# Optimization experiments

Measured on AMD Instinct MI355X. Metric: run time of the kernel, lower is better.

Reference implementation:

```python
import jax, jax.numpy as jnp
import numpy as np

B, N, C = 32, 16384, 256
D, H, S = 64, 128, 7
ITERS = 3
EPS = 1e-6
SCALE = D ** -0.5


def _ln(x, g, b):
    m = jnp.mean(x, axis=-1, keepdims=True)
    v = jnp.var(x, axis=-1, keepdims=True)
    return (x - m) / jnp.sqrt(v + 1e-5) * g + b


def _gru(x, h, Wih, Whh, bih, bhh):
    # PyTorch GRUCell: Wih/Whh are [3D, D]
    gi = x @ Wih.T + bih
    gh = h @ Whh.T + bhh
    ir, iz, inn = jnp.split(gi, 3, axis=-1)
    hr, hz, hn = jnp.split(gh, 3, axis=-1)
    r = jax.nn.sigmoid(ir + hr)
    z = jax.nn.sigmoid(iz + hz)
    n = jnp.tanh(inn + r * hn)
    return (1.0 - z) * n + z * h


def setup_inputs() -> dict:
    key = jax.random.key(0)
    ks = jax.random.split(key, 20)
    s_c = C ** -0.5
    s_d = D ** -0.5
    s_h = H ** -0.5
    p = {}
    p["inputs"] = jax.random.normal(ks[0], (B, N, C), jnp.float32)
    p["slots_mu"] = jax.random.normal(ks[1], (B, S, D), jnp.float32)
    p["ln_in_g"] = jnp.ones((C,), jnp.float32)
    p["ln_in_b"] = jnp.zeros((C,), jnp.float32)
    p["Wk"] = jax.random.normal(ks[2], (C, D), jnp.float32) * s_c
    p["Wv"] = jax.random.normal(ks[3], (C, D), jnp.float32) * s_c
    p["q_ln_g"] = jnp.ones((D,), jnp.float32)
    p["q_ln_b"] = jnp.zeros((D,), jnp.float32)
    p["Wq"] = jax.random.normal(ks[4], (D, D), jnp.float32) * s_d
    p["bq_ln_g"] = jnp.ones((D,), jnp.float32)
    p["bq_ln_b"] = jnp.zeros((D,), jnp.float32)
    p["bWq"] = jax.random.normal(ks[5], (D, D), jnp.float32) * s_d
    p["gru_Wih"] = jax.random.normal(ks[6], (3 * D, D), jnp.float32) * s_d
    p["gru_Whh"] = jax.random.normal(ks[7], (3 * D, D), jnp.float32) * s_d
    p["gru_bih"] = jnp.zeros((3 * D,), jnp.float32)
    p["gru_bhh"] = jnp.zeros((3 * D,), jnp.float32)
    p["mlp_ln_g"] = jnp.ones((D,), jnp.float32)
    p["mlp_ln_b"] = jnp.zeros((D,), jnp.float32)
    p["mlp_W1"] = jax.random.normal(ks[8], (D, H), jnp.float32) * s_d
    p["mlp_b1"] = jnp.zeros((H,), jnp.float32)
    p["mlp_W2"] = jax.random.normal(ks[9], (H, D), jnp.float32) * s_h
    p["mlp_b2"] = jnp.zeros((D,), jnp.float32)
    p["bmlp_ln_g"] = jnp.ones((D,), jnp.float32)
    p["bmlp_ln_b"] = jnp.zeros((D,), jnp.float32)
    p["bmlp_W1"] = jax.random.normal(ks[10], (D, H), jnp.float32) * s_d
    p["bmlp_b1"] = jnp.zeros((H,), jnp.float32)
    p["bmlp_W2"] = jax.random.normal(ks[11], (H, D), jnp.float32) * s_h
    p["bmlp_b2"] = jnp.zeros((D,), jnp.float32)
    return p


def reference(inputs, slots_mu, ln_in_g, ln_in_b, Wk, Wv, q_ln_g, q_ln_b, Wq,
              bq_ln_g, bq_ln_b, bWq, gru_Wih, gru_Whh, gru_bih, gru_bhh,
              mlp_ln_g, mlp_ln_b, mlp_W1, mlp_b1, mlp_W2, mlp_b2,
              bmlp_ln_g, bmlp_ln_b, bmlp_W1, bmlp_b1, bmlp_W2, bmlp_b2):
    x = _ln(inputs, ln_in_g, ln_in_b)          # [B,N,C]
    k = x @ Wk                                  # [B,N,D]
    v = x @ Wv                                  # [B,N,D]
    fg = slots_mu[:, :-1]                       # [B,S-1,D]
    bg = slots_mu[:, -1:]                       # [B,1,D]
    for _ in range(ITERS):
        fg_prev, bg_prev = fg, bg
        fq = _ln(fg, q_ln_g, q_ln_b) @ Wq
        bq = _ln(bg, bq_ln_g, bq_ln_b) @ bWq
        q = jnp.concatenate([fq, bq], axis=1)   # [B,S,D]
        logits = SCALE * jnp.einsum('bnd,bmd->bnm', k, q)  # [B,N,S]
        attn = jax.nn.softmax(logits, axis=-1) + EPS
        fa = attn[..., :-1]
        ba = attn[..., -1:]
        fa = fa / jnp.sum(fa, axis=1, keepdims=True)
        ba = ba / jnp.sum(ba, axis=1, keepdims=True)
        fu = jnp.einsum('bnm,bnd->bmd', fa, v)  # [B,S-1,D]
        bu = jnp.einsum('bnm,bnd->bmd', ba, v)  # [B,1,D]
        fg = _gru(fu.reshape(-1, D), fg_prev.reshape(-1, D),
                  gru_Wih, gru_Whh, gru_bih, gru_bhh).reshape(B, S - 1, D)
        fg = fg + (jax.nn.relu(_ln(fg, mlp_ln_g, mlp_ln_b) @ mlp_W1 + mlp_b1) @ mlp_W2 + mlp_b2)
        # NOTE: original code uses self.gru (shared) for bg, not bg_gru
        bg = _gru(bu.reshape(-1, D), bg_prev.reshape(-1, D),
                  gru_Wih, gru_Whh, gru_bih, gru_bhh).reshape(B, 1, D)
        bg = bg + (jax.nn.relu(_ln(bg, bmlp_ln_g, bmlp_ln_b) @ bmlp_W1 + bmlp_b1) @ bmlp_W2 + bmlp_b2)
    return jnp.concatenate([fg, bg], axis=1)    # [B,S,D]
```

## Files before the change

### kernel.cpp

```cpp
#include <hip/hip_runtime.h>
#include <hip/hip_bf16.h>

typedef __bf16 bf16_t;
typedef __bf16 bf16x4 __attribute__((ext_vector_type(4)));
typedef __bf16 bf16x8 __attribute__((ext_vector_type(8)));
typedef float f32x4 __attribute__((ext_vector_type(4)));

#define B_ 32
#define N_ 16384
#define C_ 256
#define D_ 64
#define ROWS_TOTAL (B_ * N_)

__device__ inline float wave_sum64(float v) {
#pragma unroll
  for (int o = 1; o < 64; o <<= 1) v += __shfl_xor(v, o);
  return v;
}

__device__ inline float sigmoidf_(float x) { return 1.0f / (1.0f + __expf(-x)); }
__device__ inline float tanhf_(float x) { return 1.0f - 2.0f / (__expf(2.0f * x) + 1.0f); }

__global__ __launch_bounds__(256) void prep_kernel(
    const float* __restrict__ Wk, const float* __restrict__ Wv,
    const float* __restrict__ Wih, const float* __restrict__ Whh,
    const float* __restrict__ slots, bf16_t* __restrict__ Wb,
    float* __restrict__ WihT, float* __restrict__ WhhT, float* __restrict__ g) {
  int i = blockIdx.x * 256 + threadIdx.x;
  if (i < 32768) {
    int j = i & 7, l = (i >> 3) & 63, t = (i >> 9) & 7, kb = i >> 12;
    int k = kb * 32 + (l >> 4) * 8 + j;
    int n = t * 16 + (l & 15);
    float v = (n < 64) ? Wk[k * 64 + n] : Wv[k * 64 + (n - 64)];
    Wb[i] = (bf16_t)v;
  } else if (i < 45056) {
    int idx = i - 32768;
    int c = idx / 192, j = idx % 192;
    WihT[idx] = Wih[j * 64 + c];
  } else if (i < 57344) {
    int idx = i - 45056;
    int c = idx / 192, j = idx % 192;
    WhhT[idx] = Whh[j * 64 + c];
  } else if (i < 71680) {
    int idx = i - 57344;
    g[idx] = slots[idx];
  }
}

__global__ __launch_bounds__(64) void qk_kernel(
    const float* __restrict__ g, const float* __restrict__ qg,
    const float* __restrict__ qb, const float* __restrict__ Wq,
    const float* __restrict__ bqg, const float* __restrict__ bqb,
    const float* __restrict__ bWq, float* __restrict__ q,
    float* __restrict__ acc, float* __restrict__ wsum) {
  __shared__ float sx[64];
  int bid = blockIdx.x, lane = threadIdx.x;
  int m = bid % 7;
  const float* lng = (m < 6) ? qg : bqg;
  const float* lnb = (m < 6) ? qb : bqb;
  const float* W = (m < 6) ? Wq : bWq;
  float gvv = g[bid * 64 + lane];
  float s = wave_sum64(gvv);
  float s2 = wave_sum64(gvv * gvv);
  float mean = s * (1.0f / 64.0f);
  float var = s2 * (1.0f / 64.0f) - mean * mean;
  float rstd = rsqrtf(var + 1e-5f);
  sx[lane] = (gvv - mean) * rstd * lng[lane] + lnb[lane];
  __syncthreads();
  float qd = 0.0f;
#pragma unroll 8
  for (int c = 0; c < 64; ++c) qd += sx[c] * W[c * 64 + lane];
  q[bid * 64 + lane] = qd;
  acc[bid * 64 + lane] = 0.0f;
  if (lane == 0) wsum[bid] = 0.0f;
}

__global__ __launch_bounds__(512) void proj_ln_kernel(
    const float* __restrict__ inp, const float* __restrict__ lng,
    const float* __restrict__ lnb, const bf16_t* __restrict__ Wb,
    bf16_t* __restrict__ kbuf, bf16_t* __restrict__ vbuf,
    const float* __restrict__ q, float* __restrict__ acc_g,
    float* __restrict__ wsum_g) {
  __shared__ bf16_t xs[128 * 256];
  __shared__ float qs[448];
  __shared__ float s_acc[448];
  __shared__ float s_w[7];
  const int tid = threadIdx.x, w = tid >> 6, lane = tid & 63;
  const int q4 = lane >> 4, lp = lane & 15;
  const long row0 = (long)blockIdx.x * 128;
  const int b = (int)(row0 >> 14);

  for (int idx = tid; idx < 448; idx += 512) {
    qs[idx] = q[b * 448 + idx];
    s_acc[idx] = 0.0f;
  }
  if (tid < 7) s_w[tid] = 0.0f;

  float4 gv[4], bv[4];
#pragma unroll
  for (int j = 0; j < 4; ++j) {
    gv[j] = *(const float4*)(lng + lp * 16 + j * 4);
    bv[j] = *(const float4*)(lnb + lp * 16 + j * 4);
  }

#pragma unroll
  for (int i = 0; i < 4; ++i) {
    int r = w * 16 + i * 4 + q4;
    const float* rp = inp + (row0 + r) * C_ + lp * 16;
    float4 x0 = *(const float4*)(rp);
    float4 x1 = *(const float4*)(rp + 4);
    float4 x2 = *(const float4*)(rp + 8);
    float4 x3 = *(const float4*)(rp + 12);
    float s = (x0.x + x0.y + x0.z + x0.w) + (x1.x + x1.y + x1.z + x1.w) +
              (x2.x + x2.y + x2.z + x2.w) + (x3.x + x3.y + x3.z + x3.w);
    float s2 = (x0.x * x0.x + x0.y * x0.y + x0.z * x0.z + x0.w * x0.w) +
               (x1.x * x1.x + x1.y * x1.y + x1.z * x1.z + x1.w * x1.w) +
               (x2.x * x2.x + x2.y * x2.y + x2.z * x2.z + x2.w * x2.w) +
               (x3.x * x3.x + x3.y * x3.y + x3.z * x3.z + x3.w * x3.w);
#pragma unroll
    for (int o = 1; o < 16; o <<= 1) {
      s += __shfl_xor(s, o);
      s2 += __shfl_xor(s2, o);
    }
    float mean = s * (1.0f / 256.0f);
    float var = s2 * (1.0f / 256.0f) - mean * mean;
    float rstd = rsqrtf(var + 1e-5f);
    bf16x8 y0, y1;
    y0[0] = (bf16_t)((x0.x - mean) * rstd * gv[0].x + bv[0].x);
    y0[1] = (bf16_t)((x0.y - mean) * rstd * gv[0].y + bv[0].y);
    y0[2] = (bf16_t)((x0.z - mean) * rstd * gv[0].z + bv[0].z);
    y0[3] = (bf16_t)((x0.w - mean) * rstd * gv[0].w + bv[0].w);
    y0[4] = (bf16_t)((x1.x - mean) * rstd * gv[1].x + bv[1].x);
    y0[5] = (bf16_t)((x1.y - mean) * rstd * gv[1].y + bv[1].y);
    y0[6] = (bf16_t)((x1.z - mean) * rstd * gv[1].z + bv[1].z);
    y0[7] = (bf16_t)((x1.w - mean) * rstd * gv[1].w + bv[1].w);
    y1[0] = (bf16_t)((x2.x - mean) * rstd * gv[2].x + bv[2].x);
    y1[1] = (bf16_t)((x2.y - mean) * rstd * gv[2].y + bv[2].y);
    y1[2] = (bf16_t)((x2.z - mean) * rstd * gv[2].z + bv[2].z);
    y1[3] = (bf16_t)((x2.w - mean) * rstd * gv[2].w + bv[2].w);
    y1[4] = (bf16_t)((x3.x - mean) * rstd * gv[3].x + bv[3].x);
    y1[5] = (bf16_t)((x3.y - mean) * rstd * gv[3].y + bv[3].y);
    y1[6] = (bf16_t)((x3.z - mean) * rstd * gv[3].z + bv[3].z);
    y1[7] = (bf16_t)((x3.w - mean) * rstd * gv[3].w + bv[3].w);
    int base = r * 32, swz = r & 31;
    *(bf16x8*)(xs + (size_t)(base + ((2 * lp) ^ swz)) * 8) = y0;
    *(bf16x8*)(xs + (size_t)(base + ((2 * lp + 1) ^ swz)) * 8) = y1;
  }
  __syncthreads();

  f32x4 acc[8];
  const f32x4 zf = {0.0f, 0.0f, 0.0f, 0.0f};
#pragma unroll
  for (int t = 0; t < 8; ++t) acc[t] = zf;

  const int r0 = w * 16 + lp;
  const int rsw = r0 & 31;
  for (int kb = 0; kb < 8; ++kb) {
    bf16x8 a = *(const bf16x8*)(xs + (size_t)(r0 * 32 + ((kb * 4 + q4) ^ rsw)) * 8);
#pragma unroll
    for (int t = 0; t < 8; ++t) {
      bf16x8 bfr = *(const bf16x8*)(Wb + (size_t)((kb * 8 + t) * 64 + lane) * 8);
      acc[t] = __builtin_amdgcn_mfma_f32_16x16x32_bf16(a, bfr, acc[t], 0, 0, 0);
    }
  }

#pragma unroll
  for (int t = 0; t < 8; ++t) {
    bf16_t* dst = (t < 4) ? kbuf : vbuf;
    int c = (t & 3) * 16 + lp;
#pragma unroll
    for (int reg = 0; reg < 4; ++reg) {
      long gr = row0 + w * 16 + q4 * 4 + reg;
      dst[gr * 64 + c] = (bf16_t)acc[t][reg];
    }
  }

  float av[7][4];
  float wa[7];
#pragma unroll
  for (int m = 0; m < 7; ++m) {
    wa[m] = 0.0f;
#pragma unroll
    for (int t = 0; t < 4; ++t) av[m][t] = 0.0f;
  }

#pragma unroll
  for (int reg = 0; reg < 4; ++reg) {
    float p[7];
#pragma unroll
    for (int m = 0; m < 7; ++m) p[m] = 0.0f;
#pragma unroll
    for (int t = 0; t < 4; ++t) {
      float at = acc[t][reg];
#pragma unroll
      for (int m = 0; m < 7; ++m) p[m] += at * qs[m * 64 + t * 16 + lp];
    }
#pragma unroll
    for (int m = 0; m < 7; ++m) {
      p[m] += __shfl_xor(p[m], 1);
      p[m] += __shfl_xor(p[m], 2);
      p[m] += __shfl_xor(p[m], 4);
      p[m] += __shfl_xor(p[m], 8);
    }
    float mx = -1e30f;
#pragma unroll
    for (int m = 0; m < 7; ++m) {
      p[m] *= 0.125f;
      mx = fmaxf(mx, p[m]);
    }
    float s = 0.0f;
#pragma unroll
    for (int m = 0; m < 7; ++m) {
      p[m] = __expf(p[m] - mx);
      s += p[m];
    }
    float inv = 1.0f / s;
#pragma unroll
    for (int m = 0; m < 7; ++m) {
      float a = p[m] * inv + 1e-6f;
      wa[m] += a;
#pragma unroll
      for (int t = 0; t < 4; ++t) av[m][t] += a * acc[4 + t][reg];
    }
  }

#pragma unroll
  for (int m = 0; m < 7; ++m) {
#pragma unroll
    for (int t = 0; t < 4; ++t) {
      av[m][t] += __shfl_xor(av[m][t], 16);
      av[m][t] += __shfl_xor(av[m][t], 32);
    }
    wa[m] += __shfl_xor(wa[m], 16);
    wa[m] += __shfl_xor(wa[m], 32);
  }
  if (q4 == 0) {
#pragma unroll
    for (int m = 0; m < 7; ++m)
#pragma unroll
      for (int t = 0; t < 4; ++t)
        atomicAdd(&s_acc[m * 64 + t * 16 + lp], av[m][t]);
  }
  if (lane == 0) {
#pragma unroll
    for (int m = 0; m < 7; ++m) atomicAdd(&s_w[m], wa[m]);
  }
  __syncthreads();
  for (int idx = tid; idx < 448; idx += 512)
    atomicAdd(&acc_g[b * 448 + idx], s_acc[idx]);
  if (tid < 7) atomicAdd(&wsum_g[b * 7 + tid], s_w[tid]);
}

__global__ __launch_bounds__(256) void attend_kernel(
    const bf16_t* __restrict__ kbuf, const bf16_t* __restrict__ vbuf,
    const float* __restrict__ q, float* __restrict__ acc,
    float* __restrict__ wsum) {
  __shared__ float qs[448];
  __shared__ float s_acc[448];
  __shared__ float s_w[7];
  int tid = threadIdx.x, w = tid >> 6, lane = tid & 63;
  int g4 = lane >> 4, lp = lane & 15;
  long chunk0 = (long)blockIdx.x * 512;
  int b = (int)(chunk0 >> 14);

  for (int idx = tid; idx < 448; idx += 256) {
    qs[idx] = q[b * 448 + idx];
    s_acc[idx] = 0.0f;
  }
  if (tid < 7) s_w[tid] = 0.0f;
  __syncthreads();

  float4 qv[7];
  const float4* qs4 = (const float4*)qs;
#pragma unroll
  for (int m = 0; m < 7; ++m) qv[m] = qs4[m * 16 + lp];

  float av[7][4];
  float wa[7];
#pragma unroll
  for (int m = 0; m < 7; ++m) {
    wa[m] = 0.0f;
#pragma unroll
    for (int j = 0; j < 4; ++j) av[m][j] = 0.0f;
  }

  for (int it = 0; it < 32; ++it) {
    long row = chunk0 + it * 16 + w * 4 + g4;
    bf16x4 kv = *(const bf16x4*)(kbuf + row * 64 + lp * 4);
    bf16x4 vv = *(const bf16x4*)(vbuf + row * 64 + lp * 4);
    float k0 = kv[0], k1 = kv[1], k2 = kv[2], k3 = kv[3];
    float lg[7];
#pragma unroll
    for (int m = 0; m < 7; ++m)
      lg[m] = k0 * qv[m].x + k1 * qv[m].y + k2 * qv[m].z + k3 * qv[m].w;
#pragma unroll
    for (int m = 0; m < 7; ++m) {
      lg[m] += __shfl_xor(lg[m], 1);
      lg[m] += __shfl_xor(lg[m], 2);
      lg[m] += __shfl_xor(lg[m], 4);
      lg[m] += __shfl_xor(lg[m], 8);
    }
    float mx = -1e30f;
#pragma unroll
    for (int m = 0; m < 7; ++m) {
      lg[m] *= 0.125f;
      mx = fmaxf(mx, lg[m]);
    }
    float e[7], s = 0.0f;
#pragma unroll
    for (int m = 0; m < 7; ++m) {
      e[m] = __expf(lg[m] - mx);
      s += e[m];
    }
    float inv = 1.0f / s;
    float v0 = vv[0], v1 = vv[1], v2 = vv[2], v3 = vv[3];
#pragma unroll
    for (int m = 0; m < 7; ++m) {
      float a = e[m] * inv + 1e-6f;
      wa[m] += a;
      av[m][0] += a * v0;
      av[m][1] += a * v1;
      av[m][2] += a * v2;
      av[m][3] += a * v3;
    }
  }

#pragma unroll
  for (int m = 0; m < 7; ++m) {
#pragma unroll
    for (int j = 0; j < 4; ++j) {
      av[m][j] += __shfl_xor(av[m][j], 16);
      av[m][j] += __shfl_xor(av[m][j], 32);
    }
    wa[m] += __shfl_xor(wa[m], 16);
    wa[m] += __shfl_xor(wa[m], 32);
  }
  if (g4 == 0) {
#pragma unroll
    for (int m = 0; m < 7; ++m)
#pragma unroll
      for (int j = 0; j < 4; ++j) atomicAdd(&s_acc[m * 64 + lp * 4 + j], av[m][j]);
  }
  if (lane == 0) {
#pragma unroll
    for (int m = 0; m < 7; ++m) atomicAdd(&s_w[m], wa[m]);
  }
  __syncthreads();
  for (int idx = tid; idx < 448; idx += 256) atomicAdd(&acc[b * 448 + idx], s_acc[idx]);
  if (tid < 7) atomicAdd(&wsum[b * 7 + tid], s_w[tid]);
}

__global__ __launch_bounds__(192) void update_kernel(
    const float* __restrict__ acc, const float* __restrict__ wsum,
    const float* __restrict__ g, const float* __restrict__ WihT,
    const float* __restrict__ WhhT, const float* __restrict__ bih,
    const float* __restrict__ bhh, const float* __restrict__ mlg,
    const float* __restrict__ mlb, const float* __restrict__ mW1,
    const float* __restrict__ mb1, const float* __restrict__ mW2,
    const float* __restrict__ mb2, const float* __restrict__ bmlg,
    const float* __restrict__ bmlb, const float* __restrict__ bW1,
    const float* __restrict__ bb1, const float* __restrict__ bW2,
    const float* __restrict__ bb2, float* __restrict__ gout,
    const float* __restrict__ qg, const float* __restrict__ qb,
    const float* __restrict__ Wq, const float* __restrict__ bqg,
    const float* __restrict__ bqb, const float* __restrict__ bWq,
    float* __restrict__ qout, float* __restrict__ accz,
    float* __restrict__ wsz, int write_q) {
  __shared__ float fu[64], hp[64], gi[192], gh[192], h2[64], xb[64], a1[128], go[64];
  int tid = threadIdx.x, bid = blockIdx.x, m = bid % 7;

  const float *lg_, *lb_, *W1_, *b1_, *W2_, *b2_;
  if (m < 6) { lg_ = mlg; lb_ = mlb; W1_ = mW1; b1_ = mb1; W2_ = mW2; b2_ = mb2; }
  else       { lg_ = bmlg; lb_ = bmlb; W1_ = bW1; b1_ = bb1; W2_ = bW2; b2_ = bb2; }

  if (tid < 64) {
    float wv = wsum[bid];
    fu[tid] = acc[bid * 64 + tid] / wv;
    hp[tid] = g[bid * 64 + tid];
  }
  __syncthreads();

  {
    int j = tid;
    float a = bih[j], bsum = bhh[j];
    for (int c = 0; c < 64; ++c) {
      a += fu[c] * WihT[c * 192 + j];
      bsum += hp[c] * WhhT[c * 192 + j];
    }
    gi[j] = a;
    gh[j] = bsum;
  }
  __syncthreads();

  if (tid < 64) {
    int d = tid;
    float r = sigmoidf_(gi[d] + gh[d]);
    float z = sigmoidf_(gi[64 + d] + gh[64 + d]);
    float n = tanhf_(gi[128 + d] + r * gh[128 + d]);
    float h = (1.0f - z) * n + z * hp[d];
    h2[d] = h;
    float s = wave_sum64(h);
    float s2 = wave_sum64(h * h);
    float mean = s * (1.0f / 64.0f);
    float var = s2 * (1.0f / 64.0f) - mean * mean;
    xb[d] = (h - mean) * rsqrtf(var + 1e-5f) * lg_[d] + lb_[d];
  }
  __syncthreads();

  if (tid < 128) {
    int hh = tid;
    float a = b1_[hh];
    for (int c = 0; c < 64; ++c) a += xb[c] * W1_[c * 128 + hh];
    a1[hh] = fmaxf(a, 0.0f);
  }
  __syncthreads();

  if (tid < 64) {
    int d = tid;
    float o = b2_[d];
    for (int hh = 0; hh < 128; ++hh) o += a1[hh] * W2_[hh * 64 + d];
    float res = h2[d] + o;
    gout[bid * 64 + d] = res;
    go[d] = res;
  }
  __syncthreads();

  if (write_q) {
    if (tid < 64) {
      const float* qlng = (m < 6) ? qg : bqg;
      const float* qlnb = (m < 6) ? qb : bqb;
      const float* W = (m < 6) ? Wq : bWq;
      float gvv = go[tid];
      float s = wave_sum64(gvv);
      float s2 = wave_sum64(gvv * gvv);
      float mean = s * (1.0f / 64.0f);
      float var = s2 * (1.0f / 64.0f) - mean * mean;
      xb[tid] = (gvv - mean) * rsqrtf(var + 1e-5f) * qlng[tid] + qlnb[tid];
      __syncwarp();
      float qd = 0.0f;
      const float* Wl = W;
#pragma unroll 8
      for (int c = 0; c < 64; ++c) qd += xb[c] * Wl[c * 64 + tid];
      qout[bid * 64 + tid] = qd;
      accz[bid * 64 + tid] = 0.0f;
      if (tid == 0) wsz[bid] = 0.0f;
    }
  }
}

extern "C" void kernel_launch(void* const* d_in, const int* in_sizes, int n_in,
                              void* d_out, int out_size, void* d_ws, size_t ws_size,
                              hipStream_t stream) {
  const float* inputs   = (const float*)d_in[0];
  const float* slots_mu = (const float*)d_in[1];
  const float* ln_in_g  = (const float*)d_in[2];
  const float* ln_in_b  = (const float*)d_in[3];
  const float* Wk       = (const float*)d_in[4];
  const float* Wv       = (const float*)d_in[5];
  const float* q_ln_g   = (const float*)d_in[6];
  const float* q_ln_b   = (const float*)d_in[7];
  const float* Wq       = (const float*)d_in[8];
  const float* bq_ln_g  = (const float*)d_in[9];
  const float* bq_ln_b  = (const float*)d_in[10];
  const float* bWq      = (const float*)d_in[11];
  const float* gru_Wih  = (const float*)d_in[12];
  const float* gru_Whh  = (const float*)d_in[13];
  const float* gru_bih  = (const float*)d_in[14];
  const float* gru_bhh  = (const float*)d_in[15];
  const float* mlp_ln_g = (const float*)d_in[16];
  const float* mlp_ln_b = (const float*)d_in[17];
  const float* mlp_W1   = (const float*)d_in[18];
  const float* mlp_b1   = (const float*)d_in[19];
  const float* mlp_W2   = (const float*)d_in[20];
  const float* mlp_b2   = (const float*)d_in[21];
  const float* bmlp_ln_g = (const float*)d_in[22];
  const float* bmlp_ln_b = (const float*)d_in[23];
  const float* bmlp_W1  = (const float*)d_in[24];
  const float* bmlp_b1  = (const float*)d_in[25];
  const float* bmlp_W2  = (const float*)d_in[26];
  const float* bmlp_b2  = (const float*)d_in[27];
  float* out = (float*)d_out;

  char* ws = (char*)d_ws;
  const size_t KV_BYTES = (size_t)ROWS_TOTAL * 64 * 2;
  bf16_t* kbuf = (bf16_t*)ws;
  bf16_t* vbuf = (bf16_t*)(ws + KV_BYTES);
  bf16_t* Wb   = (bf16_t*)(ws + 2 * KV_BYTES);
  float* WihT  = (float*)(ws + 2 * KV_BYTES + 65536);
  float* WhhT  = (float*)(ws + 2 * KV_BYTES + 65536 + 49152);
  float* gbuf  = (float*)(ws + 2 * KV_BYTES + 65536 + 2 * 49152);
  float* qbuf  = (float*)(ws + 2 * KV_BYTES + 65536 + 2 * 49152 + 57344);
  float* accb  = (float*)(ws + 2 * KV_BYTES + 65536 + 2 * 49152 + 2 * 57344);
  float* wsumb = (float*)(ws + 2 * KV_BYTES + 65536 + 2 * 49152 + 3 * 57344);

  prep_kernel<<<280, 256, 0, stream>>>(Wk, Wv, gru_Wih, gru_Whh, slots_mu, Wb,
                                       WihT, WhhT, gbuf);
  qk_kernel<<<224, 64, 0, stream>>>(gbuf, q_ln_g, q_ln_b, Wq, bq_ln_g, bq_ln_b,
                                    bWq, qbuf, accb, wsumb);
  proj_ln_kernel<<<ROWS_TOTAL / 128, 512, 0, stream>>>(
      inputs, ln_in_g, ln_in_b, Wb, kbuf, vbuf, qbuf, accb, wsumb);
  for (int it = 0; it < 3; ++it) {
    if (it > 0)
      attend_kernel<<<ROWS_TOTAL / 512, 256, 0, stream>>>(kbuf, vbuf, qbuf,
                                                          accb, wsumb);
    update_kernel<<<224, 192, 0, stream>>>(
        accb, wsumb, gbuf, WihT, WhhT, gru_bih, gru_bhh, mlp_ln_g, mlp_ln_b,
        mlp_W1, mlp_b1, mlp_W2, mlp_b2, bmlp_ln_g, bmlp_ln_b, bmlp_W1, bmlp_b1,
        bmlp_W2, bmlp_b2, (it == 2) ? out : gbuf, q_ln_g, q_ln_b, Wq, bq_ln_g,
        bq_ln_b, bWq, qbuf, accb, wsumb, (it < 2) ? 1 : 0);
  }
}
```

Before: 1.059 ms.

## Replace global atomics with per-chunk partial sums and fuse q init into prep

Proj and attend kernels now write per-block partial accumulators to a workspace slab instead of atomically adding into global buffers. The update kernel reduces these partials over chunks, which removes the need to zero the accumulators. The separate qk kernel is folded into the prep kernel as extra blocks, dropping one launch. The cost is extra partial-buffer traffic and a serial loop over up to 128 chunks in update. Global atomic contention is small here, so the gain is mostly one fewer launch.

```diff
diff --git a/kernel.cpp b/kernel.cpp
--- a/kernel.cpp
+++ b/kernel.cpp
@@ -11,6 +11,7 @@
 #define C_ 256
 #define D_ 64
 #define ROWS_TOTAL (B_ * N_)
+#define MAXCH 128
 
 __device__ inline float wave_sum64(float v) {
 #pragma unroll
@@ -24,63 +25,61 @@
 __global__ __launch_bounds__(256) void prep_kernel(
     const float* __restrict__ Wk, const float* __restrict__ Wv,
     const float* __restrict__ Wih, const float* __restrict__ Whh,
-    const float* __restrict__ slots, bf16_t* __restrict__ Wb,
-    float* __restrict__ WihT, float* __restrict__ WhhT, float* __restrict__ g) {
-  int i = blockIdx.x * 256 + threadIdx.x;
-  if (i < 32768) {
-    int j = i & 7, l = (i >> 3) & 63, t = (i >> 9) & 7, kb = i >> 12;
-    int k = kb * 32 + (l >> 4) * 8 + j;
-    int n = t * 16 + (l & 15);
-    float v = (n < 64) ? Wk[k * 64 + n] : Wv[k * 64 + (n - 64)];
-    Wb[i] = (bf16_t)v;
-  } else if (i < 45056) {
-    int idx = i - 32768;
-    int c = idx / 192, j = idx % 192;
-    WihT[idx] = Wih[j * 64 + c];
-  } else if (i < 57344) {
-    int idx = i - 45056;
-    int c = idx / 192, j = idx % 192;
-    WhhT[idx] = Whh[j * 64 + c];
-  } else if (i < 71680) {
-    int idx = i - 57344;
-    g[idx] = slots[idx];
-  }
-}
-
-__global__ __launch_bounds__(64) void qk_kernel(
-    const float* __restrict__ g, const float* __restrict__ qg,
+    const float* __restrict__ slots, const float* __restrict__ qg,
     const float* __restrict__ qb, const float* __restrict__ Wq,
     const float* __restrict__ bqg, const float* __restrict__ bqb,
-    const float* __restrict__ bWq, float* __restrict__ q,
-    float* __restrict__ acc, float* __restrict__ wsum) {
-  __shared__ float sx[64];
-  int bid = blockIdx.x, lane = threadIdx.x;
-  int m = bid % 7;
-  const float* lng = (m < 6) ? qg : bqg;
-  const float* lnb = (m < 6) ? qb : bqb;
-  const float* W = (m < 6) ? Wq : bWq;
-  float gvv = g[bid * 64 + lane];
-  float s = wave_sum64(gvv);
-  float s2 = wave_sum64(gvv * gvv);
-  float mean = s * (1.0f / 64.0f);
-  float var = s2 * (1.0f / 64.0f) - mean * mean;
-  float rstd = rsqrtf(var + 1e-5f);
-  sx[lane] = (gvv - mean) * rstd * lng[lane] + lnb[lane];
-  __syncthreads();
-  float qd = 0.0f;
+    const float* __restrict__ bWq, bf16_t* __restrict__ Wb,
+    float* __restrict__ WihT, float* __restrict__ WhhT, float* __restrict__ g,
+    float* __restrict__ q) {
+  __shared__ float sx[256];
+  if (blockIdx.x < 280) {
+    int i = blockIdx.x * 256 + threadIdx.x;
+    if (i < 32768) {
+      int j = i & 7, l = (i >> 3) & 63, t = (i >> 9) & 7, kb = i >> 12;
+      int k = kb * 32 + (l >> 4) * 8 + j;
+      int n = t * 16 + (l & 15);
+      float v = (n < 64) ? Wk[k * 64 + n] : Wv[k * 64 + (n - 64)];
+      Wb[i] = (bf16_t)v;
+    } else if (i < 45056) {
+      int idx = i - 32768;
+      int c = idx / 192, j = idx % 192;
+      WihT[idx] = Wih[j * 64 + c];
+    } else if (i < 57344) {
+      int idx = i - 45056;
+      int c = idx / 192, j = idx % 192;
+      WhhT[idx] = Whh[j * 64 + c];
+    } else if (i < 71680) {
+      int idx = i - 57344;
+      g[idx] = slots[idx];
+    }
+  } else {
+    int w = threadIdx.x >> 6, lane = threadIdx.x & 63;
+    int bid = (blockIdx.x - 280) * 4 + w;
+    int m = bid % 7;
+    const float* lng = (m < 6) ? qg : bqg;
+    const float* lnb = (m < 6) ? qb : bqb;
+    const float* W = (m < 6) ? Wq : bWq;
+    float gvv = slots[bid * 64 + lane];
+    float s = wave_sum64(gvv);
+    float s2 = wave_sum64(gvv * gvv);
+    float mean = s * (1.0f / 64.0f);
+    float var = s2 * (1.0f / 64.0f) - mean * mean;
+    float rstd = rsqrtf(var + 1e-5f);
+    sx[w * 64 + lane] = (gvv - mean) * rstd * lng[lane] + lnb[lane];
+    __syncthreads();
+    float qd = 0.0f;
 #pragma unroll 8
-  for (int c = 0; c < 64; ++c) qd += sx[c] * W[c * 64 + lane];
-  q[bid * 64 + lane] = qd;
-  acc[bid * 64 + lane] = 0.0f;
-  if (lane == 0) wsum[bid] = 0.0f;
+    for (int c = 0; c < 64; ++c) qd += sx[w * 64 + c] * W[c * 64 + lane];
+    q[bid * 64 + lane] = qd;
+  }
 }
 
 __global__ __launch_bounds__(512) void proj_ln_kernel(
     const float* __restrict__ inp, const float* __restrict__ lng,
     const float* __restrict__ lnb, const bf16_t* __restrict__ Wb,
     bf16_t* __restrict__ kbuf, bf16_t* __restrict__ vbuf,
-    const float* __restrict__ q, float* __restrict__ acc_g,
-    float* __restrict__ wsum_g) {
+    const float* __restrict__ q, float* __restrict__ pacc,
+    float* __restrict__ pw) {
   __shared__ bf16_t xs[128 * 256];
   __shared__ float qs[448];
   __shared__ float s_acc[448];
@@ -88,7 +87,8 @@
   const int tid = threadIdx.x, w = tid >> 6, lane = tid & 63;
   const int q4 = lane >> 4, lp = lane & 15;
   const long row0 = (long)blockIdx.x * 128;
-  const int b = (int)(row0 >> 14);
+  const int b = blockIdx.x >> 7;
+  const int cb = blockIdx.x & 127;
 
   for (int idx = tid; idx < 448; idx += 512) {
     qs[idx] = q[b * 448 + idx];
@@ -246,22 +246,23 @@
     for (int m = 0; m < 7; ++m) atomicAdd(&s_w[m], wa[m]);
   }
   __syncthreads();
-  for (int idx = tid; idx < 448; idx += 512)
-    atomicAdd(&acc_g[b * 448 + idx], s_acc[idx]);
-  if (tid < 7) atomicAdd(&wsum_g[b * 7 + tid], s_w[tid]);
+  float* pa = pacc + (size_t)(b * MAXCH + cb) * 448;
+  for (int idx = tid; idx < 448; idx += 512) pa[idx] = s_acc[idx];
+  if (tid < 7) pw[(b * MAXCH + cb) * 7 + tid] = s_w[tid];
 }
 
 __global__ __launch_bounds__(256) void attend_kernel(
     const bf16_t* __restrict__ kbuf, const bf16_t* __restrict__ vbuf,
-    const float* __restrict__ q, float* __restrict__ acc,
-    float* __restrict__ wsum) {
+    const float* __restrict__ q, float* __restrict__ pacc,
+    float* __restrict__ pw) {
   __shared__ float qs[448];
   __shared__ float s_acc[448];
   __shared__ float s_w[7];
   int tid = threadIdx.x, w = tid >> 6, lane = tid & 63;
   int g4 = lane >> 4, lp = lane & 15;
   long chunk0 = (long)blockIdx.x * 512;
-  int b = (int)(chunk0 >> 14);
+  int b = blockIdx.x >> 5;
+  int cb = blockIdx.x & 31;
 
   for (int idx = tid; idx < 448; idx += 256) {
     qs[idx] = q[b * 448 + idx];
@@ -346,12 +347,13 @@
     for (int m = 0; m < 7; ++m) atomicAdd(&s_w[m], wa[m]);
   }
   __syncthreads();
-  for (int idx = tid; idx < 448; idx += 256) atomicAdd(&acc[b * 448 + idx], s_acc[idx]);
-  if (tid < 7) atomicAdd(&wsum[b * 7 + tid], s_w[tid]);
+  float* pa = pacc + (size_t)(b * MAXCH + cb) * 448;
+  for (int idx = tid; idx < 448; idx += 256) pa[idx] = s_acc[idx];
+  if (tid < 7) pw[(b * MAXCH + cb) * 7 + tid] = s_w[tid];
 }
 
 __global__ __launch_bounds__(192) void update_kernel(
-    const float* __restrict__ acc, const float* __restrict__ wsum,
+    const float* __restrict__ pacc, const float* __restrict__ pw, int nch,
     const float* __restrict__ g, const float* __restrict__ WihT,
     const float* __restrict__ WhhT, const float* __restrict__ bih,
     const float* __restrict__ bhh, const float* __restrict__ mlg,
@@ -364,18 +366,25 @@
     const float* __restrict__ qg, const float* __restrict__ qb,
     const float* __restrict__ Wq, const float* __restrict__ bqg,
     const float* __restrict__ bqb, const float* __restrict__ bWq,
-    float* __restrict__ qout, float* __restrict__ accz,
-    float* __restrict__ wsz, int write_q) {
+    float* __restrict__ qout, int write_q) {
   __shared__ float fu[64], hp[64], gi[192], gh[192], h2[64], xb[64], a1[128], go[64];
-  int tid = threadIdx.x, bid = blockIdx.x, m = bid % 7;
+  int tid = threadIdx.x, bid = blockIdx.x, m = bid % 7, b = bid / 7;
 
   const float *lg_, *lb_, *W1_, *b1_, *W2_, *b2_;
   if (m < 6) { lg_ = mlg; lb_ = mlb; W1_ = mW1; b1_ = mb1; W2_ = mW2; b2_ = mb2; }
   else       { lg_ = bmlg; lb_ = bmlb; W1_ = bW1; b1_ = bb1; W2_ = bW2; b2_ = bb2; }
 
   if (tid < 64) {
-    float wv = wsum[bid];
-    fu[tid] = acc[bid * 64 + tid] / wv;
+    const float* pa = pacc + (size_t)b * MAXCH * 448 + m * 64 + tid;
+    float s = 0.0f;
+#pragma unroll 8
+    for (int c = 0; c < nch; ++c) s += pa[(size_t)c * 448];
+    const float* pwp = pw + (size_t)b * MAXCH * 7 + m;
+    float wp = 0.0f;
+    if (tid < nch) wp = pwp[tid * 7];
+    if (tid + 64 < nch) wp += pwp[(tid + 64) * 7];
+    float wv = wave_sum64(wp);
+    fu[tid] = s / wv;
     hp[tid] = g[bid * 64 + tid];
   }
   __syncthreads();
@@ -438,12 +447,9 @@
       xb[tid] = (gvv - mean) * rsqrtf(var + 1e-5f) * qlng[tid] + qlnb[tid];
       __syncwarp();
       float qd = 0.0f;
-      const float* Wl = W;
 #pragma unroll 8
-      for (int c = 0; c < 64; ++c) qd += xb[c] * Wl[c * 64 + tid];
+      for (int c = 0; c < 64; ++c) qd += xb[c] * W[c * 64 + tid];
       qout[bid * 64 + tid] = qd;
-      accz[bid * 64 + tid] = 0.0f;
-      if (tid == 0) wsz[bid] = 0.0f;
     }
   }
 }
@@ -483,30 +489,30 @@
 
   char* ws = (char*)d_ws;
   const size_t KV_BYTES = (size_t)ROWS_TOTAL * 64 * 2;
-  bf16_t* kbuf = (bf16_t*)ws;
-  bf16_t* vbuf = (bf16_t*)(ws + KV_BYTES);
-  bf16_t* Wb   = (bf16_t*)(ws + 2 * KV_BYTES);
-  float* WihT  = (float*)(ws + 2 * KV_BYTES + 65536);
-  float* WhhT  = (float*)(ws + 2 * KV_BYTES + 65536 + 49152);
-  float* gbuf  = (float*)(ws + 2 * KV_BYTES + 65536 + 2 * 49152);
-  float* qbuf  = (float*)(ws + 2 * KV_BYTES + 65536 + 2 * 49152 + 57344);
-  float* accb  = (float*)(ws + 2 * KV_BYTES + 65536 + 2 * 49152 + 2 * 57344);
-  float* wsumb = (float*)(ws + 2 * KV_BYTES + 65536 + 2 * 49152 + 3 * 57344);
-
-  prep_kernel<<<280, 256, 0, stream>>>(Wk, Wv, gru_Wih, gru_Whh, slots_mu, Wb,
-                                       WihT, WhhT, gbuf);
-  qk_kernel<<<224, 64, 0, stream>>>(gbuf, q_ln_g, q_ln_b, Wq, bq_ln_g, bq_ln_b,
-                                    bWq, qbuf, accb, wsumb);
+  size_t off = 0;
+  bf16_t* kbuf = (bf16_t*)(ws + off); off += KV_BYTES;
+  bf16_t* vbuf = (bf16_t*)(ws + off); off += KV_BYTES;
+  bf16_t* Wb   = (bf16_t*)(ws + off); off += 65536;
+  float* WihT  = (float*)(ws + off);  off += 49152;
+  float* WhhT  = (float*)(ws + off);  off += 49152;
+  float* gbuf  = (float*)(ws + off);  off += 57344;
+  float* qbuf  = (float*)(ws + off);  off += 57344;
+  float* pacc  = (float*)(ws + off);  off += (size_t)B_ * MAXCH * 448 * 4;
+  float* pw    = (float*)(ws + off);  off += (size_t)B_ * MAXCH * 7 * 4;
+
+  prep_kernel<<<336, 256, 0, stream>>>(Wk, Wv, gru_Wih, gru_Whh, slots_mu,
+                                       q_ln_g, q_ln_b, Wq, bq_ln_g, bq_ln_b,
+                                       bWq, Wb, WihT, WhhT, gbuf, qbuf);
   proj_ln_kernel<<<ROWS_TOTAL / 128, 512, 0, stream>>>(
-      inputs, ln_in_g, ln_in_b, Wb, kbuf, vbuf, qbuf, accb, wsumb);
+      inputs, ln_in_g, ln_in_b, Wb, kbuf, vbuf, qbuf, pacc, pw);
   for (int it = 0; it < 3; ++it) {
     if (it > 0)
       attend_kernel<<<ROWS_TOTAL / 512, 256, 0, stream>>>(kbuf, vbuf, qbuf,
-                                                          accb, wsumb);
+                                                          pacc, pw);
     update_kernel<<<224, 192, 0, stream>>>(
-        accb, wsumb, gbuf, WihT, WhhT, gru_bih, gru_bhh, mlp_ln_g, mlp_ln_b,
-        mlp_W1, mlp_b1, mlp_W2, mlp_b2, bmlp_ln_g, bmlp_ln_b, bmlp_W1, bmlp_b1,
-        bmlp_W2, bmlp_b2, (it == 2) ? out : gbuf, q_ln_g, q_ln_b, Wq, bq_ln_g,
-        bq_ln_b, bWq, qbuf, accb, wsumb, (it < 2) ? 1 : 0);
+        pacc, pw, (it == 0) ? 128 : 32, gbuf, WihT, WhhT, gru_bih, gru_bhh,
+        mlp_ln_g, mlp_ln_b, mlp_W1, mlp_b1, mlp_W2, mlp_b2, bmlp_ln_g,
+        bmlp_ln_b, bmlp_W1, bmlp_b1, bmlp_W2, bmlp_b2, (it == 2) ? out : gbuf,
+        q_ln_g, q_ln_b, Wq, bq_ln_g, bq_ln_b, bWq, qbuf, (it < 2) ? 1 : 0);
   }
 }
```

Result: no change. 1.070 ms (+1.1%).
